# Kernel optimization log

Hardware: AMD Instinct MI355X
Metric: run time of the kernel (lower is better)

Reference implementation:

```python
import jax, jax.numpy as jnp
import numpy as np

T, B, E, H = 1024, 2, 1024, 16
D = E // H  # head_dim = 64
R = 2 * T - 1  # relative position range


def setup_inputs() -> dict:
    key = jax.random.key(0)
    ks = jax.random.split(key, 8)
    std = (2.0 / (E + E)) ** 0.5  # matches nn.init.normal_ std in reset_parameters
    return {
        "x": jax.random.normal(ks[0], (T, B, E), jnp.float32),
        "pos": jax.random.normal(ks[1], (R, 1, E), jnp.float32),
        "in_proj_weight": jax.random.normal(ks[2], (3 * E, E), jnp.float32) * std,
        "in_proj_bias": jnp.zeros((3 * E,), jnp.float32),
        "pos_proj_weight": jax.random.normal(ks[3], (E, E), jnp.float32) * std,
        "pos_proj_bias": jnp.zeros((E,), jnp.float32),
        "out_proj_weight": jax.random.normal(ks[4], (E, E), jnp.float32) * std,
        "out_proj_bias": jnp.zeros((E,), jnp.float32),
        "r_w_bias": jax.random.normal(ks[5], (H, D), jnp.float32) * 0.02,
        "r_r_bias": jax.random.normal(ks[6], (H, D), jnp.float32) * 0.02,
    }


def _rel_shift(x):
    """Transformer-XL relative shift. x: [b, h, q, r] -> shifted [b, h, q, r]."""
    b, h, q, r = x.shape
    zp = jnp.zeros((b, h, q, 1), x.dtype)
    xp = jnp.concatenate([zp, x], axis=3)          # [b, h, q, r+1]
    xp = xp.reshape(b, h, r + 1, q)[:, :, 1:, :]   # drop first row
    return xp.reshape(b, h, q, r)


def reference(x, pos, in_proj_weight, in_proj_bias, pos_proj_weight,
              pos_proj_bias, out_proj_weight, out_proj_bias, r_w_bias, r_r_bias):
    t, b, e = x.shape
    h, d = r_w_bias.shape
    # fused QKV projection: [T, B, 3E]
    qkv = x @ in_proj_weight.T + in_proj_bias
    q, k, v = jnp.split(qkv, 3, axis=-1)
    q = q.reshape(t, b, h, d)
    k = k.reshape(t, b, h, d)
    v = v.reshape(t, b, h, d)
    # position projection: [R, 1, E] -> [R, h, d]
    p = (pos @ pos_proj_weight.T + pos_proj_bias).reshape(-1, h, d)
    scale = 1.0 / jnp.sqrt(jnp.asarray(d, x.dtype))
    # content score AC: (q + r_w_bias) @ k^T
    ac = jnp.einsum('tbhd,sbhd->bhts', q + r_w_bias, k)
    # position score BD: (q + r_r_bias) @ pos^T, then relative shift
    bd = jnp.einsum('tbhd,rhd->bhtr', q + r_r_bias, p)
    bd = _rel_shift(bd)[..., :t]                    # keep klen columns
    attn = jax.nn.softmax((ac + bd) * scale, axis=-1)  # [b, h, t, s]
    ctx = jnp.einsum('bhts,sbhd->tbhd', attn, v).reshape(t, b, e)
    return ctx @ out_proj_weight.T + out_proj_bias
```

## Files before the change

kernel.cpp:

```cpp
#include <hip/hip_runtime.h>
#include <hip/hip_bf16.h>

#define TT 1024
#define BB 2
#define EE 1024
#define HH 16
#define DD 64
#define RR 2047
#define TB (TT * BB)
#define E3 (3 * EE)

#define AS1 __attribute__((address_space(1)))
#define AS3 __attribute__((address_space(3)))

typedef __attribute__((ext_vector_type(4))) float f32x4;
typedef __attribute__((ext_vector_type(8))) short s16x8;

static __device__ __forceinline__ short f2bf(float x) {
  unsigned u = __builtin_bit_cast(unsigned, x);
  unsigned r = (u + 0x7FFFu + ((u >> 16) & 1u)) >> 16;
  return (short)r;
}
static __device__ __forceinline__ float bf2f(short x) {
  unsigned u = ((unsigned)(unsigned short)x) << 16;
  return __builtin_bit_cast(float, u);
}
static __device__ __forceinline__ float bperm(int idx, float v) {
  return __builtin_bit_cast(float,
      __builtin_amdgcn_ds_bpermute(idx, __builtin_bit_cast(int, v)));
}

__global__ __launch_bounds__(256) void cvt_all(
    const float* __restrict__ x, const float* __restrict__ in_w,
    const float* __restrict__ pos, const float* __restrict__ pos_w,
    const float* __restrict__ out_w,
    short* __restrict__ xb, short* __restrict__ inwb, short* __restrict__ posb,
    short* __restrict__ poswb, short* __restrict__ outwb) {
  const long M1 = 1 << 20;
  long off = (long)(blockIdx.x * 256 + threadIdx.x) * 8;
  const float* src; short* dst; long nsrc;
  if (off < 2 * M1)      { src = x;     dst = xb;    nsrc = 2 * M1; }
  else if (off < 5 * M1) { off -= 2 * M1; src = in_w;  dst = inwb;  nsrc = 3 * M1; }
  else if (off < 7 * M1) { off -= 5 * M1; src = pos;   dst = posb;  nsrc = (long)RR * EE; }
  else if (off < 8 * M1) { off -= 7 * M1; src = pos_w; dst = poswb; nsrc = M1; }
  else                   { off -= 8 * M1; src = out_w; dst = outwb; nsrc = M1; }
  s16x8 o;
  if (off + 8 <= nsrc) {
    f32x4 a = *(const f32x4*)&src[off];
    f32x4 c = *(const f32x4*)&src[off + 4];
    #pragma unroll
    for (int j = 0; j < 4; ++j) { o[j] = f2bf(a[j]); o[4 + j] = f2bf(c[j]); }
  } else {
    #pragma unroll
    for (int j = 0; j < 8; ++j) o[j] = 0;
  }
  *(s16x8*)&dst[off] = o;
}

#define GBK 32

template <int BM, int BN, int WR, int WC, int OUT_BF16>
__device__ __forceinline__ void gemm_body(
    const short* __restrict__ A, const short* __restrict__ W,
    const float* __restrict__ bias, void* __restrict__ Cout,
    int M, int N, int K, int m0, int n0) {
  __shared__ __align__(16) short lA[2][BM * GBK];
  __shared__ __align__(16) short lB[2][BN * GBK];
  constexpr int MT = BM / WR / 16;
  constexpr int NT = BN / WC / 16;
  constexpr int ACH = BM * 4 / 256;
  constexpr int BCH = BN * 4 / 256;

  const int tid = threadIdx.x;
  const int lane = tid & 63;
  const int wv = tid >> 6;
  const int g = lane >> 4, cc = lane & 15;
  const int wr = wv / WC, wc = wv % WC;

  f32x4 acc[MT][NT];
  #pragma unroll
  for (int i = 0; i < MT; ++i)
    #pragma unroll
    for (int j = 0; j < NT; ++j) acc[i][j] = (f32x4){0.f, 0.f, 0.f, 0.f};

  auto stage = [&](int kk, int buf) {
    #pragma unroll
    for (int s = 0; s < ACH; ++s) {
      int c = s * 256 + tid;
      int row = c >> 2, slot = c & 3;
      int k8 = slot ^ (row & 3);
      __builtin_amdgcn_global_load_lds(
          (const AS1 void*)(A + (size_t)(m0 + row) * K + kk + k8 * 8),
          (AS3 void*)&lA[buf][c * 8], 16, 0, 0);
    }
    #pragma unroll
    for (int s = 0; s < BCH; ++s) {
      int c = s * 256 + tid;
      int row = c >> 2, slot = c & 3;
      int k8 = slot ^ (row & 3);
      __builtin_amdgcn_global_load_lds(
          (const AS1 void*)(W + (size_t)(n0 + row) * K + kk + k8 * 8),
          (AS3 void*)&lB[buf][c * 8], 16, 0, 0);
    }
  };

  int cur = 0;
  const int nt = K / GBK;
  stage(0, 0);

  #pragma unroll 1
  for (int t = 0; t < nt; ++t) {
    __syncthreads();
    if (t + 1 < nt) stage((t + 1) * GBK, cur ^ 1);

    s16x8 af[MT], bf[NT];
    #pragma unroll
    for (int mt = 0; mt < MT; ++mt) {
      int row = (BM / WR) * wr + 16 * mt + cc;
      af[mt] = *(const s16x8*)&lA[cur][row * GBK + ((g ^ (row & 3)) * 8)];
    }
    #pragma unroll
    for (int ntc = 0; ntc < NT; ++ntc) {
      int col = (BN / WC) * wc + 16 * ntc + cc;
      bf[ntc] = *(const s16x8*)&lB[cur][col * GBK + ((g ^ (col & 3)) * 8)];
    }
    #pragma unroll
    for (int mt = 0; mt < MT; ++mt)
      #pragma unroll
      for (int ntc = 0; ntc < NT; ++ntc)
        acc[mt][ntc] = __builtin_amdgcn_mfma_f32_16x16x32_bf16(
            af[mt], bf[ntc], acc[mt][ntc], 0, 0, 0);
    cur ^= 1;
  }

  #pragma unroll
  for (int ntc = 0; ntc < NT; ++ntc) {
    int col = n0 + (BN / WC) * wc + 16 * ntc + cc;
    float bv = bias[col - n0 + n0];
    bv = bias[col];
    #pragma unroll
    for (int mt = 0; mt < MT; ++mt)
      #pragma unroll
      for (int r = 0; r < 4; ++r) {
        int rowg = m0 + (BM / WR) * wr + 16 * mt + 4 * g + r;
        float val = acc[mt][ntc][r] + bv;
        if (OUT_BF16)
          ((short*)Cout)[(size_t)rowg * N + col] = f2bf(val);
        else
          ((float*)Cout)[(size_t)rowg * N + col] = val;
      }
  }
}

__global__ __launch_bounds__(256) void gemm_qkv_pos(
    const short* __restrict__ xb, const short* __restrict__ inwb,
    const float* __restrict__ in_b, short* __restrict__ qkvb,
    const short* __restrict__ posb, const short* __restrict__ poswb,
    const float* __restrict__ pos_b, short* __restrict__ pb) {
  const int bid = blockIdx.x;
  const short *A, *W; const float* bias; short* C; int N, m0, n0;
  if (bid < 384) {
    A = xb; W = inwb; bias = in_b; C = qkvb; N = E3;
    n0 = (bid % 24) * 128; m0 = (bid / 24) * 128;
  } else {
    const int i = bid - 384;
    A = posb; W = poswb; bias = pos_b; C = pb; N = EE;
    n0 = (i % 8) * 128; m0 = (i / 8) * 128;
  }
  gemm_body<128, 128, 2, 2, 1>(A, W, bias, C, TB, N, EE, m0, n0);
}

__global__ __launch_bounds__(256) void gemm_out(
    const short* __restrict__ ctxb, const short* __restrict__ outwb,
    const float* __restrict__ out_b, float* __restrict__ out) {
  gemm_body<128, 64, 4, 1, 0>(ctxb, outwb, out_b, out, TB, EE, EE,
                              blockIdx.y * 128, blockIdx.x * 64);
}

__global__ __launch_bounds__(256) void transpose_v(
    const short* __restrict__ qkvb, short* __restrict__ vT) {
  __shared__ short tile[64][72];
  const int tid = threadIdx.x;
  const int kt = blockIdx.x;
  const int bh = blockIdx.y;
  const int b = bh >> 4, h = bh & 15;
  const int j = tid >> 2;
  const int cg = (tid & 3) * 16;
  const short* src = qkvb + (size_t)((kt * 64 + j) * BB + b) * E3 + 2 * EE + h * DD + cg;
  *(s16x8*)&tile[j][cg]     = *(const s16x8*)src;
  *(s16x8*)&tile[j][cg + 8] = *(const s16x8*)(src + 8);
  __syncthreads();
  short* dst = vT + (size_t)(bh * DD + j) * TT + kt * 64 + cg;
  s16x8 o0, o1;
  #pragma unroll
  for (int m = 0; m < 8; ++m) { o0[m] = tile[cg + m][j]; o1[m] = tile[cg + 8 + m][j]; }
  *(s16x8*)dst       = o0;
  *(s16x8*)(dst + 8) = o1;
}

__global__ __launch_bounds__(512, 4) void rel_attn_mfma8(
    const short* __restrict__ qkvb,
    const short* __restrict__ pb,
    const short* __restrict__ vT,
    const float* __restrict__ rwb,
    const float* __restrict__ rrb,
    short* __restrict__ ctxb) {
  __shared__ __align__(16) char arena[76800];

  const int tid = threadIdx.x;
  const int wv = tid >> 6;
  const int qsub = wv & 3, ksub = wv >> 2;
  const int lane = tid & 63;
  const int g = lane >> 4, cc = lane & 15;

  const int bid = blockIdx.x;
  const int bh = (bid & 7) * 4 + (bid >> 7);
  const int qx = (bid >> 3) & 15;
  const int iq0 = qx * 64;
  const int b = bh >> 4, h = bh & 15;
  const int hoff = h * DD;

  short* sPm = (short*)(arena + 65536 + wv * 1280);

  s16x8 qw[2], qr[2];
  #pragma unroll
  for (int kh = 0; kh < 2; ++kh) {
    const int d0 = 32 * kh + 8 * g;
    const short* qp = qkvb + (size_t)((iq0 + 16 * qsub + cc) * BB + b) * E3 + hoff + d0;
    const float* rw = rwb + hoff + d0;
    const float* rr = rrb + hoff + d0;
    s16x8 qv = *(const s16x8*)qp;
    #pragma unroll
    for (int j = 0; j < 8; ++j) {
      float q = bf2f(qv[j]);
      qw[kh][j] = f2bf((q + rw[j]) * 0.125f);
      qr[kh][j] = f2bf((q + rr[j]) * 0.125f);
    }
  }

  f32x4 O[4];
  #pragma unroll
  for (int dt = 0; dt < 4; ++dt) O[dt] = (f32x4){0.f, 0.f, 0.f, 0.f};
  float mrun[4], lpart[4];
  #pragma unroll
  for (int r = 0; r < 4; ++r) { mrun[r] = -1e30f; lpart[r] = 0.f; }

#define STAGE(t_, bufb_)                                                       \
  {                                                                            \
    const int j0s = (t_) * 64;                                                 \
    const int gmins = j0s - iq0 + 960;                                         \
    const int row = tid >> 3, c8 = tid & 7;                                    \
    const int swz = (c8 ^ (row & 7)) * 8;                                      \
    __builtin_amdgcn_global_load_lds(                                          \
        (const AS1 void*)(qkvb + (size_t)((j0s + row) * BB + b) * E3 + EE + hoff + swz), \
        (AS3 void*)((bufb_) + tid * 16), 16, 0, 0);                            \
    __builtin_amdgcn_global_load_lds(                                          \
        (const AS1 void*)(vT + (size_t)(bh * DD + row) * TT + j0s + swz),      \
        (AS3 void*)((bufb_) + 8192 + tid * 16), 16, 0, 0);                     \
    _Pragma("unroll")                                                          \
    for (int s2 = 0; s2 < 2; ++s2) {                                           \
      const int c2 = tid + 512 * s2;                                           \
      const int prow = c2 >> 3, pc8 = c2 & 7;                                  \
      const int pswz = (pc8 ^ (prow & 7)) * 8;                                 \
      __builtin_amdgcn_global_load_lds(                                        \
          (const AS1 void*)(pb + (size_t)(gmins + prow) * EE + hoff + pswz),   \
          (AS3 void*)((bufb_) + 16384 + c2 * 16), 16, 0, 0);                   \
    }                                                                          \
  }

  int cur = 0;
  STAGE(0, arena);

  #pragma unroll 1
  for (int t = 0; t < 16; ++t) {
    __syncthreads();
    char* bufc = arena + cur * 32768;
    if (t + 1 < 16) STAGE(t + 1, arena + (cur ^ 1) * 32768);

    short* ldsK = (short*)bufc;
    short* ldsV = (short*)(bufc + 8192);
    short* ldsP = (short*)(bufc + 16384);

    s16x8 kf[2][2];
    #pragma unroll
    for (int ct = 0; ct < 2; ++ct)
      #pragma unroll
      for (int kh = 0; kh < 2; ++kh) {
        const int row = 32 * ksub + 16 * ct + cc;
        kf[ct][kh] = *(const s16x8*)&ldsK[row * 64 + (((g + 4 * kh) ^ (row & 7)) * 8)];
      }

    f32x4 S[2];
    #pragma unroll
    for (int ct = 0; ct < 2; ++ct) {
      S[ct] = (f32x4){0.f, 0.f, 0.f, 0.f};
      #pragma unroll
      for (int kh = 0; kh < 2; ++kh)
        S[ct] = __builtin_amdgcn_mfma_f32_16x16x32_bf16(qw[kh], kf[ct][kh], S[ct], 0, 0, 0);
    }

    const int bbase = 32 * ksub - 16 * qsub + 48;
    f32x4 bt[3];
    #pragma unroll
    for (int ut = 0; ut < 3; ++ut) {
      const int rel = bbase + 16 * ut + cc;
      bt[ut] = (f32x4){0.f, 0.f, 0.f, 0.f};
      #pragma unroll
      for (int kh = 0; kh < 2; ++kh) {
        s16x8 pf = *(const s16x8*)&ldsP[rel * 64 + (((g + 4 * kh) ^ (rel & 7)) * 8)];
        bt[ut] = __builtin_amdgcn_mfma_f32_16x16x32_bf16(qr[kh], pf, bt[ut], 0, 0, 0);
      }
    }
    #pragma unroll
    for (int r = 0; r < 4; ++r) {
      const int usub = cc + 15 - 4 * g - r;
      const int idx = ((lane & 48) | (usub & 15)) << 2;
      const float va = bperm(idx, bt[0][r]);
      const float vb = bperm(idx, bt[1][r]);
      const float vc = bperm(idx, bt[2][r]);
      const bool hi = usub >= 16;
      S[0][r] += hi ? vb : va;
      S[1][r] += hi ? vc : vb;
    }

    float mx[4];
    #pragma unroll
    for (int r = 0; r < 4; ++r) mx[r] = fmaxf(S[0][r], S[1][r]);
    const bool need = (mx[0] > mrun[0]) || (mx[1] > mrun[1]) ||
                      (mx[2] > mrun[2]) || (mx[3] > mrun[3]);
    if (__any(need)) {
      #pragma unroll
      for (int msk = 1; msk < 16; msk <<= 1)
        #pragma unroll
        for (int r = 0; r < 4; ++r) mx[r] = fmaxf(mx[r], __shfl_xor(mx[r], msk, 64));
      #pragma unroll
      for (int r = 0; r < 4; ++r) {
        const float mn = fmaxf(mrun[r], mx[r]);
        const float f = __expf(mrun[r] - mn);
        mrun[r] = mn;
        lpart[r] *= f;
        #pragma unroll
        for (int dt = 0; dt < 4; ++dt) O[dt][r] *= f;
      }
    }
    #pragma unroll
    for (int r = 0; r < 4; ++r) {
      S[0][r] = __expf(S[0][r] - mrun[r]);
      S[1][r] = __expf(S[1][r] - mrun[r]);
      lpart[r] += S[0][r] + S[1][r];
    }

    #pragma unroll
    for (int ct = 0; ct < 2; ++ct)
      #pragma unroll
      for (int r = 0; r < 4; ++r)
        sPm[(4 * g + r) * 40 + 16 * ct + cc] = f2bf(S[ct][r]);

    s16x8 pa = *(const s16x8*)&sPm[cc * 40 + 8 * g];

    #pragma unroll
    for (int dt = 0; dt < 4; ++dt) {
      const int row = 16 * dt + cc;
      s16x8 vf = *(const s16x8*)&ldsV[row * 64 + (((4 * ksub + g) ^ (row & 7)) * 8)];
      O[dt] = __builtin_amdgcn_mfma_f32_16x16x32_bf16(pa, vf, O[dt], 0, 0, 0);
    }
    cur ^= 1;
  }
#undef STAGE

  #pragma unroll
  for (int msk = 1; msk < 16; msk <<= 1)
    #pragma unroll
    for (int r = 0; r < 4; ++r) lpart[r] += __shfl_xor(lpart[r], msk, 64);

  __syncthreads();

  float* sOw = (float*)(arena + wv * 4352);
  #pragma unroll
  for (int dt = 0; dt < 4; ++dt)
    #pragma unroll
    for (int r = 0; r < 4; ++r)
      sOw[(4 * g + r) * 68 + 16 * dt + cc] = O[dt][r];
  float* sML = (float*)(arena + 75776);
  if (cc == 0) {
    #pragma unroll
    for (int r = 0; r < 4; ++r) {
      sML[wv * 32 + (4 * g + r)] = mrun[r];
      sML[wv * 32 + 16 + (4 * g + r)] = lpart[r];
    }
  }
  __syncthreads();

  const int ii = tid >> 3;
  const int ii_l = ii & 15;
  const int w0 = ii >> 4, w1 = w0 + 4;
  const int c0 = (tid & 7) * 8;
  const float m0 = sML[w0 * 32 + ii_l], l0 = sML[w0 * 32 + 16 + ii_l];
  const float m1 = sML[w1 * 32 + ii_l], l1 = sML[w1 * 32 + 16 + ii_l];
  const float M = fmaxf(m0, m1);
  const float f0 = __expf(m0 - M), f1 = __expf(m1 - M);
  const float rinv = 1.0f / (f0 * l0 + f1 * l1);
  const float* sO0 = (const float*)(arena + w0 * 4352);
  const float* sO1 = (const float*)(arena + w1 * 4352);
  s16x8 ov;
  #pragma unroll
  for (int jj = 0; jj < 8; ++jj) {
    const float val = (f0 * sO0[ii_l * 68 + c0 + jj] + f1 * sO1[ii_l * 68 + c0 + jj]) * rinv;
    ov[jj] = f2bf(val);
  }
  *(s16x8*)(ctxb + (size_t)((iq0 + ii) * BB + b) * EE + hoff + c0) = ov;
}

extern "C" void kernel_launch(void* const* d_in, const int* in_sizes, int n_in,
                              void* d_out, int out_size, void* d_ws, size_t ws_size,
                              hipStream_t stream) {
  const float* x      = (const float*)d_in[0];
  const float* pos    = (const float*)d_in[1];
  const float* in_w   = (const float*)d_in[2];
  const float* in_b   = (const float*)d_in[3];
  const float* pos_w  = (const float*)d_in[4];
  const float* pos_b  = (const float*)d_in[5];
  const float* out_w  = (const float*)d_in[6];
  const float* out_b  = (const float*)d_in[7];
  const float* r_w    = (const float*)d_in[8];
  const float* r_r    = (const float*)d_in[9];
  float* out = (float*)d_out;

  const size_t M1 = 1024 * 1024;
  short* xb    = (short*)d_ws;
  short* inwb  = xb    + 2 * M1;
  short* posb  = inwb  + 3 * M1;
  short* poswb = posb  + 2 * M1;
  short* outwb = poswb + 1 * M1;
  short* qkvb  = outwb + 1 * M1;
  short* pb    = qkvb  + 6 * M1;
  short* ctxb  = pb    + 2 * M1;
  short* vTb   = ctxb  + 2 * M1;

  cvt_all<<<dim3(4608), dim3(256), 0, stream>>>(
      x, in_w, pos, pos_w, out_w, xb, inwb, posb, poswb, outwb);

  gemm_qkv_pos<<<dim3(512), dim3(256), 0, stream>>>(
      xb, inwb, in_b, qkvb, posb, poswb, pos_b, pb);

  transpose_v<<<dim3(TT / 64, BB * HH), dim3(256), 0, stream>>>(qkvb, vTb);

  rel_attn_mfma8<<<dim3(512), dim3(512), 0, stream>>>(
      qkvb, pb, vTb, r_w, r_r, ctxb);

  gemm_out<<<dim3(EE / 64, TB / 128), dim3(256), 0, stream>>>(
      ctxb, outwb, out_b, out);
}
```

Baseline: 109.5 us.

## Fuse V transpose into QKV GEMM epilogue and ring-buffer position tiles

```diff
diff --git a/kernel.cpp b/kernel.cpp
--- a/kernel.cpp
+++ b/kernel.cpp
@@ -63,7 +63,8 @@
 __device__ __forceinline__ void gemm_body(
     const short* __restrict__ A, const short* __restrict__ W,
     const float* __restrict__ bias, void* __restrict__ Cout,
-    int M, int N, int K, int m0, int n0) {
+    int M, int N, int K, int m0, int n0,
+    short* __restrict__ vtout, int vtflag) {
   __shared__ __align__(16) short lA[2][BM * GBK];
   __shared__ __align__(16) short lB[2][BN * GBK];
   constexpr int MT = BM / WR / 16;
@@ -136,18 +137,25 @@
   #pragma unroll
   for (int ntc = 0; ntc < NT; ++ntc) {
     int col = n0 + (BN / WC) * wc + 16 * ntc + cc;
-    float bv = bias[col - n0 + n0];
-    bv = bias[col];
+    float bv = bias[col];
     #pragma unroll
     for (int mt = 0; mt < MT; ++mt)
       #pragma unroll
       for (int r = 0; r < 4; ++r) {
         int rowg = m0 + (BM / WR) * wr + 16 * mt + 4 * g + r;
         float val = acc[mt][ntc][r] + bv;
-        if (OUT_BF16)
-          ((short*)Cout)[(size_t)rowg * N + col] = f2bf(val);
-        else
+        if (OUT_BF16) {
+          if (vtflag) {
+            const int cv = col - 2048;
+            const int hh = cv >> 6, dd = cv & 63;
+            vtout[((size_t)((rowg & 1) * 16 + hh) * 64 + dd) * TT + (rowg >> 1)] =
+                f2bf(val);
+          } else {
+            ((short*)Cout)[(size_t)rowg * N + col] = f2bf(val);
+          }
+        } else {
           ((float*)Cout)[(size_t)rowg * N + col] = val;
+        }
       }
   }
 }
@@ -156,56 +164,38 @@
     const short* __restrict__ xb, const short* __restrict__ inwb,
     const float* __restrict__ in_b, short* __restrict__ qkvb,
     const short* __restrict__ posb, const short* __restrict__ poswb,
-    const float* __restrict__ pos_b, short* __restrict__ pb) {
+    const float* __restrict__ pos_b, short* __restrict__ pb,
+    short* __restrict__ vTb) {
   const int bid = blockIdx.x;
-  const short *A, *W; const float* bias; short* C; int N, m0, n0;
+  const short *A, *W; const float* bias; short* C; int N, m0, n0, vtf;
   if (bid < 384) {
     A = xb; W = inwb; bias = in_b; C = qkvb; N = E3;
     n0 = (bid % 24) * 128; m0 = (bid / 24) * 128;
+    vtf = (n0 >= 2048) ? 1 : 0;
   } else {
     const int i = bid - 384;
     A = posb; W = poswb; bias = pos_b; C = pb; N = EE;
     n0 = (i % 8) * 128; m0 = (i / 8) * 128;
-  }
-  gemm_body<128, 128, 2, 2, 1>(A, W, bias, C, TB, N, EE, m0, n0);
+    vtf = 0;
+  }
+  gemm_body<128, 128, 2, 2, 1>(A, W, bias, C, TB, N, EE, m0, n0, vTb, vtf);
 }
 
 __global__ __launch_bounds__(256) void gemm_out(
     const short* __restrict__ ctxb, const short* __restrict__ outwb,
     const float* __restrict__ out_b, float* __restrict__ out) {
   gemm_body<128, 64, 4, 1, 0>(ctxb, outwb, out_b, out, TB, EE, EE,
-                              blockIdx.y * 128, blockIdx.x * 64);
-}
-
-__global__ __launch_bounds__(256) void transpose_v(
-    const short* __restrict__ qkvb, short* __restrict__ vT) {
-  __shared__ short tile[64][72];
-  const int tid = threadIdx.x;
-  const int kt = blockIdx.x;
-  const int bh = blockIdx.y;
-  const int b = bh >> 4, h = bh & 15;
-  const int j = tid >> 2;
-  const int cg = (tid & 3) * 16;
-  const short* src = qkvb + (size_t)((kt * 64 + j) * BB + b) * E3 + 2 * EE + h * DD + cg;
-  *(s16x8*)&tile[j][cg]     = *(const s16x8*)src;
-  *(s16x8*)&tile[j][cg + 8] = *(const s16x8*)(src + 8);
-  __syncthreads();
-  short* dst = vT + (size_t)(bh * DD + j) * TT + kt * 64 + cg;
-  s16x8 o0, o1;
-  #pragma unroll
-  for (int m = 0; m < 8; ++m) { o0[m] = tile[cg + m][j]; o1[m] = tile[cg + 8 + m][j]; }
-  *(s16x8*)dst       = o0;
-  *(s16x8*)(dst + 8) = o1;
-}
-
-__global__ __launch_bounds__(512, 4) void rel_attn_mfma8(
+                              blockIdx.y * 128, blockIdx.x * 64, nullptr, 0);
+}
+
+__global__ __launch_bounds__(512, 4) void rel_attn_mfma9(
     const short* __restrict__ qkvb,
     const short* __restrict__ pb,
     const short* __restrict__ vT,
     const float* __restrict__ rwb,
     const float* __restrict__ rrb,
     short* __restrict__ ctxb) {
-  __shared__ __align__(16) char arena[76800];
+  __shared__ __align__(16) char arena[68608];
 
   const int tid = threadIdx.x;
   const int wv = tid >> 6;
@@ -219,8 +209,9 @@
   const int iq0 = qx * 64;
   const int b = bh >> 4, h = bh & 15;
   const int hoff = h * DD;
-
-  short* sPm = (short*)(arena + 65536 + wv * 1280);
+  const int n0p = 15 - qx;
+
+  short* sPm = (short*)(arena + 57344 + wv * 1280);
 
   s16x8 qw[2], qr[2];
   #pragma unroll
@@ -245,41 +236,43 @@
   #pragma unroll
   for (int r = 0; r < 4; ++r) { mrun[r] = -1e30f; lpart[r] = 0.f; }
 
-#define STAGE(t_, bufb_)                                                       \
+#define STAGE_KV(t_, buf_)                                                     \
   {                                                                            \
     const int j0s = (t_) * 64;                                                 \
-    const int gmins = j0s - iq0 + 960;                                         \
     const int row = tid >> 3, c8 = tid & 7;                                    \
     const int swz = (c8 ^ (row & 7)) * 8;                                      \
     __builtin_amdgcn_global_load_lds(                                          \
         (const AS1 void*)(qkvb + (size_t)((j0s + row) * BB + b) * E3 + EE + hoff + swz), \
-        (AS3 void*)((bufb_) + tid * 16), 16, 0, 0);                            \
+        (AS3 void*)(arena + (buf_) * 8192 + tid * 16), 16, 0, 0);              \
     __builtin_amdgcn_global_load_lds(                                          \
         (const AS1 void*)(vT + (size_t)(bh * DD + row) * TT + j0s + swz),      \
-        (AS3 void*)((bufb_) + 8192 + tid * 16), 16, 0, 0);                     \
-    _Pragma("unroll")                                                          \
-    for (int s2 = 0; s2 < 2; ++s2) {                                           \
-      const int c2 = tid + 512 * s2;                                           \
-      const int prow = c2 >> 3, pc8 = c2 & 7;                                  \
-      const int pswz = (pc8 ^ (prow & 7)) * 8;                                 \
-      __builtin_amdgcn_global_load_lds(                                        \
-          (const AS1 void*)(pb + (size_t)(gmins + prow) * EE + hoff + pswz),   \
-          (AS3 void*)((bufb_) + 16384 + c2 * 16), 16, 0, 0);                   \
-    }                                                                          \
+        (AS3 void*)(arena + 16384 + (buf_) * 8192 + tid * 16), 16, 0, 0);      \
+  }
+#define STAGE_P(p_)                                                            \
+  {                                                                            \
+    const int row = tid >> 3, c8 = tid & 7;                                    \
+    const int swz = (c8 ^ (row & 7)) * 8;                                      \
+    __builtin_amdgcn_global_load_lds(                                          \
+        (const AS1 void*)(pb + (size_t)((p_) * 64 + row) * EE + hoff + swz),   \
+        (AS3 void*)(arena + 32768 + ((p_) % 3) * 8192 + tid * 16), 16, 0, 0);  \
   }
 
   int cur = 0;
-  STAGE(0, arena);
+  int sl0 = n0p % 3, sl1 = (n0p + 1) % 3;
+  STAGE_KV(0, 0);
+  STAGE_P(n0p);
+  STAGE_P(n0p + 1);
 
   #pragma unroll 1
   for (int t = 0; t < 16; ++t) {
     __syncthreads();
-    char* bufc = arena + cur * 32768;
-    if (t + 1 < 16) STAGE(t + 1, arena + (cur ^ 1) * 32768);
-
-    short* ldsK = (short*)bufc;
-    short* ldsV = (short*)(bufc + 8192);
-    short* ldsP = (short*)(bufc + 16384);
+    if (t + 1 < 16) {
+      STAGE_KV(t + 1, cur ^ 1);
+      STAGE_P(n0p + t + 2);
+    }
+
+    short* ldsK = (short*)(arena + cur * 8192);
+    short* ldsV = (short*)(arena + 16384 + cur * 8192);
 
     s16x8 kf[2][2];
     #pragma unroll
@@ -304,10 +297,13 @@
     #pragma unroll
     for (int ut = 0; ut < 3; ++ut) {
       const int rel = bbase + 16 * ut + cc;
+      const int rr = rel & 63;
+      const short* pp_ = (const short*)(arena + 32768 +
+                                        ((rel >= 64) ? sl1 : sl0) * 8192);
       bt[ut] = (f32x4){0.f, 0.f, 0.f, 0.f};
       #pragma unroll
       for (int kh = 0; kh < 2; ++kh) {
-        s16x8 pf = *(const s16x8*)&ldsP[rel * 64 + (((g + 4 * kh) ^ (rel & 7)) * 8)];
+        s16x8 pf = *(const s16x8*)&pp_[rr * 64 + (((g + 4 * kh) ^ (rr & 7)) * 8)];
         bt[ut] = __builtin_amdgcn_mfma_f32_16x16x32_bf16(qr[kh], pf, bt[ut], 0, 0, 0);
       }
     }
@@ -364,9 +360,14 @@
       s16x8 vf = *(const s16x8*)&ldsV[row * 64 + (((4 * ksub + g) ^ (row & 7)) * 8)];
       O[dt] = __builtin_amdgcn_mfma_f32_16x16x32_bf16(pa, vf, O[dt], 0, 0, 0);
     }
+
     cur ^= 1;
-  }
-#undef STAGE
+    const int sln = (sl1 + 1) - (((sl1 + 1) >= 3) ? 3 : 0);
+    sl0 = sl1;
+    sl1 = sln;
+  }
+#undef STAGE_KV
+#undef STAGE_P
 
   #pragma unroll
   for (int msk = 1; msk < 16; msk <<= 1)
@@ -381,7 +382,7 @@
     #pragma unroll
     for (int r = 0; r < 4; ++r)
       sOw[(4 * g + r) * 68 + 16 * dt + cc] = O[dt][r];
-  float* sML = (float*)(arena + 75776);
+  float* sML = (float*)(arena + 67584);
   if (cc == 0) {
     #pragma unroll
     for (int r = 0; r < 4; ++r) {
@@ -441,11 +442,9 @@
       x, in_w, pos, pos_w, out_w, xb, inwb, posb, poswb, outwb);
 
   gemm_qkv_pos<<<dim3(512), dim3(256), 0, stream>>>(
-      xb, inwb, in_b, qkvb, posb, poswb, pos_b, pb);
-
-  transpose_v<<<dim3(TT / 64, BB * HH), dim3(256), 0, stream>>>(qkvb, vTb);
-
-  rel_attn_mfma8<<<dim3(512), dim3(512), 0, stream>>>(
+      xb, inwb, in_b, qkvb, posb, poswb, pos_b, pb, vTb);
+
+  rel_attn_mfma9<<<dim3(512), dim3(512), 0, stream>>>(
       qkvb, pb, vTb, r_w, r_r, ctxb);
 
   gemm_out<<<dim3(EE / 64, TB / 128), dim3(256), 0, stream>>>(
```

After: 110.8 us. No clear change (+1.1%).
